# Performance work log

Measured on AMD Instinct MI355X. Metric: run time of the kernel, lower is better.

## Reference

```python
import jax, jax.numpy as jnp
import numpy as np

B, T, D, H = 2, 2048, 1024, 16
DK = D // H


def setup_inputs() -> dict:
    key = jax.random.key(0)
    ks = jax.random.split(key, 9)
    s = 1.0 / np.sqrt(D)
    x = jax.random.normal(ks[0], (B, T, D), dtype=jnp.float32)
    # causal mask (1 = attend, 0 = masked), broadcast over batch and heads
    mask = jnp.tril(jnp.ones((T, T), dtype=jnp.int32))[None, None, :, :]
    Wq = jax.random.uniform(ks[1], (D, D), jnp.float32, -s, s)
    bq = jax.random.uniform(ks[2], (D,), jnp.float32, -s, s)
    Wk = jax.random.uniform(ks[3], (D, D), jnp.float32, -s, s)
    bk = jax.random.uniform(ks[4], (D,), jnp.float32, -s, s)
    Wv = jax.random.uniform(ks[5], (D, D), jnp.float32, -s, s)
    bv = jax.random.uniform(ks[6], (D,), jnp.float32, -s, s)
    Wo = jax.random.uniform(ks[7], (D, D), jnp.float32, -s, s)
    bo = jax.random.uniform(ks[8], (D,), jnp.float32, -s, s)
    return {"x": x, "mask": mask, "Wq": Wq, "bq": bq, "Wk": Wk, "bk": bk,
            "Wv": Wv, "bv": bv, "Wo": Wo, "bo": bo}


def reference(x, mask, Wq, bq, Wk, bk, Wv, bv, Wo, bo):
    # nn.Linear: y = x @ W.T + b
    q = (x @ Wq.T + bq).reshape(B, T, H, DK).transpose(0, 2, 1, 3)  # [B,H,T,DK]
    k = (x @ Wk.T + bk).reshape(B, T, H, DK).transpose(0, 2, 1, 3)
    v = (x @ Wv.T + bv).reshape(B, T, H, DK).transpose(0, 2, 1, 3)
    scores = jnp.einsum('bhqd,bhkd->bhqk', q, k) / np.sqrt(DK).astype(np.float32)
    scores = jnp.where(mask == 0, -jnp.inf, scores)
    attn = jax.nn.softmax(scores, axis=-1)
    out = jnp.einsum('bhqk,bhkd->bhqd', attn, v)  # [B,H,T,DK]
    out = out.transpose(0, 2, 1, 3).reshape(B, T, D)
    return out @ Wo.T + bo
```

## Files before the change

### kernel.cpp

```cpp
#include <hip/hip_runtime.h>

typedef unsigned short u16;
typedef unsigned int u32;
typedef unsigned long long u64;
typedef __attribute__((ext_vector_type(8))) short short8;
typedef __attribute__((ext_vector_type(4))) float f32x4;

#define B_ 2
#define T_ 2048
#define H_ 16
#define DK_ 64
#define QSCALE 0.18033688011112042f

__device__ __forceinline__ u16 f2bf(float f){
  unsigned u = __float_as_uint(f);
  return (u16)((u + 0x7fffu + ((u >> 16) & 1u)) >> 16);
}

__device__ __forceinline__ u32 cvtpk(float lo, float hi){
  u32 r;
  asm("v_cvt_pk_bf16_f32 %0, %1, %2" : "=v"(r) : "v"(lo), "v"(hi));
  return r;
}

#if defined(__has_builtin)
#if __has_builtin(__builtin_amdgcn_global_load_lds)
#define HAS_GLLDS 1
#endif
#if __has_builtin(__builtin_amdgcn_exp2f)
#define EXP2(x) __builtin_amdgcn_exp2f(x)
#endif
#endif
#ifndef EXP2
#define EXP2(x) __expf(0.69314718056f * (x))
#endif

#ifdef HAS_GLLDS
__device__ __forceinline__ void gl_lds16(const u16* g, u16* l){
  __builtin_amdgcn_global_load_lds(
      (__attribute__((address_space(1))) void*)(void*)g,
      (__attribute__((address_space(3))) void*)(void*)l, 16, 0, 0);
}
#endif

__global__ __launch_bounds__(256) void conv_all(
    const float* __restrict__ x, const float* __restrict__ wq, const float* __restrict__ wk,
    const float* __restrict__ wv, const float* __restrict__ wo,
    u16* __restrict__ xb, u16* __restrict__ wqb, u16* __restrict__ wkb,
    u16* __restrict__ wvb, u16* __restrict__ wob)
{
  int gid = blockIdx.x * 256 + threadIdx.x;
  const float* src; u16* dst; int off;
  if (gid < 1048576){ src = x; dst = xb; off = gid; }
  else {
    int t = gid - 1048576; int s = t >> 18; off = t & 262143;
    src = (s==0)?wq:((s==1)?wk:((s==2)?wv:wo));
    dst = (s==0)?wqb:((s==1)?wkb:((s==2)?wvb:wob));
  }
  float4 v = ((const float4*)src)[off];
  u64 r = (u64)f2bf(v.x) | ((u64)f2bf(v.y)<<16) | ((u64)f2bf(v.z)<<32) | ((u64)f2bf(v.w)<<48);
  ((u64*)dst)[off] = r;
}

template<int QKV>
__global__ __launch_bounds__(256, 3) void gemm_k3(
    const u16* __restrict__ A,
    const u16* __restrict__ W0, const u16* __restrict__ W1, const u16* __restrict__ W2,
    const float* __restrict__ b0, const float* __restrict__ b1, const float* __restrict__ b2,
    void* __restrict__ o0, void* __restrict__ o1, void* __restrict__ o2)
{
  __shared__ u16 As[2][128*32];
  __shared__ u16 Bs[2][128*32];
  const int tid = threadIdx.x;
  const int sel = QKV ? (blockIdx.x >> 3) : 0;
  const int n0 = (blockIdx.x & 7) * 128;
  const int m0 = blockIdx.y * 128;
  const u16* Bw = (sel==0)?W0:((sel==1)?W1:W2);
  const float* bias = (sel==0)?b0:((sel==1)?b1:b2);
  const int w = tid>>6, l = tid&63;
  const int lr = l&15, lg = l>>4;
  const int wm = (w&1)*64, wn = (w>>1)*64;
  const u16* Ab = A  + (size_t)m0*1024 + (size_t)(l>>2)*1024 + (l&3)*8;
  const u16* Bb = Bw + (size_t)n0*1024 + (size_t)(l>>2)*1024 + (l&3)*8;
  f32x4 acc[4][4] = {};

#define G_STAGE(k0, pb) do {                                                    \
    _Pragma("unroll")                                                           \
    for (int i_ = 0; i_ < 2; ++i_){                                             \
      int c_ = w*2 + i_;                                                        \
      G_STAGE_ONE(Ab, As, c_, k0, pb); G_STAGE_ONE(Bb, Bs, c_, k0, pb);         \
    } } while(0)
#ifdef HAS_GLLDS
#define G_STAGE_ONE(SRC, DST, c_, k0, pb) \
    gl_lds16(SRC + (size_t)(16*(c_))*1024 + (k0), &DST[pb][(c_)*512])
#else
#define G_STAGE_ONE(SRC, DST, c_, k0, pb) \
    *(uint4*)&DST[pb][(c_)*512 + l*8] = *(const uint4*)(SRC + (size_t)(16*(c_))*1024 + (k0))
#endif

  G_STAGE(0, 0);
  __syncthreads();
  for (int it = 0; it < 32; ++it){
    const int pb = it & 1;
    if (it < 31) G_STAGE((it+1)*32, pb^1);
    short8 af[4], bf[4];
#pragma unroll
    for (int mi=0;mi<4;++mi) af[mi] = *(const short8*)&As[pb][(wm+16*mi+lr)*32 + 8*lg];
#pragma unroll
    for (int ni=0;ni<4;++ni) bf[ni] = *(const short8*)&Bs[pb][(wn+16*ni+lr)*32 + 8*lg];
#pragma unroll
    for (int mi=0;mi<4;++mi)
#pragma unroll
      for (int ni=0;ni<4;++ni)
        acc[mi][ni] = __builtin_amdgcn_mfma_f32_16x16x32_bf16(af[mi], bf[ni], acc[mi][ni], 0,0,0);
    __syncthreads();
  }

  float bv[4];
#pragma unroll
  for (int ni=0;ni<4;++ni) bv[ni] = bias[n0+wn+16*ni+lr];
  void* C = QKV ? ((sel==0)?o0:((sel==1)?o1:o2)) : o0;
#pragma unroll
  for (int mi=0;mi<4;++mi)
#pragma unroll
    for (int r=0;r<4;++r){
      const int trow = m0 + wm + 16*mi + 4*lg + r;
#pragma unroll
      for (int ni=0;ni<4;++ni){
        float v = acc[mi][ni][r] + bv[ni];
        int n = n0 + wn + 16*ni + lr;
        if (!QKV){
          ((float*)C)[(size_t)trow*1024 + n] = v;
        } else if (sel == 0){
          ((u16*)C)[(size_t)trow*1024 + n] = f2bf(v * QSCALE);
        } else if (sel == 1){
          int nsw = (n & ~63) | ((n & 63) ^ ((trow & 7) << 3));
          ((u16*)C)[(size_t)trow*1024 + nsw] = f2bf(v);
        } else {
          ((u16*)C)[(size_t)trow*1024 + n] = f2bf(v);
        }
      }
    }
#undef G_STAGE
#undef G_STAGE_ONE
}

__global__ __launch_bounds__(256) void transpose_v_k(const u16* __restrict__ V,
                                                     u16* __restrict__ VT){
  __shared__ u16 L[64 * 72];
  const int tid = threadIdx.x;
  const int tc = blockIdx.x, h = blockIdx.y, b = blockIdx.z;
#pragma unroll
  for (int p = 0; p < 2; ++p){
    int row = (tid >> 3) + 32 * p, g = tid & 7;
    *(uint4*)&L[row * 72 + g * 8] =
        *(const uint4*)(V + ((size_t)(b * T_ + tc * 64 + row) * H_ + h) * DK_ + g * 8);
  }
  __syncthreads();
#pragma unroll
  for (int p = 0; p < 2; ++p){
    int d = tid >> 2, g8 = (tid & 3) + 4 * p;
    union { uint4 u; u16 s[8]; } tv;
#pragma unroll
    for (int i = 0; i < 8; ++i){
      int pp = 8 * g8 + i;
      int tl = 16 * (pp & 3) + (pp >> 2);
      tv.s[i] = L[tl * 72 + d];
    }
    *(uint4*)(VT + ((size_t)(b * H_ + h) * DK_ + d) * T_ + tc * 64 + ((8 * g8) ^ ((d & 7) << 3))) = tv.u;
  }
}

__global__ __launch_bounds__(256, 2) void attn_v3(
    const u16* __restrict__ Q, const u16* __restrict__ K,
    const u16* __restrict__ VT, u16* __restrict__ O)
{
  __shared__ u16 Ks[2][64*64];
  __shared__ u16 VTs[2][64*64];
  __shared__ u16 Ps[4][32*72];
  const int tid = threadIdx.x;
  const int w = tid>>6, l = tid&63;
  const int lr = l&15, lg = l>>4;
  const int h = blockIdx.y, b = blockIdx.z;
  const int qtb = (b==0) ? blockIdx.x : (15 - blockIdx.x);
  const int q0 = qtb * 128;
  const int wrow0 = q0 + w*32;
  const int sl_r = l>>3, sl_c = (l&7)*8;
  const size_t kbase = ((size_t)(b*T_) * H_ + h) * DK_;
  const size_t vbase = (size_t)(b*H_ + h) * DK_ * (size_t)T_;

#define A_STAGE(kt, pb) do {                                                       \
    _Pragma("unroll")                                                              \
    for (int p_=0;p_<2;++p_){                                                      \
      int r0_ = 8*w + 32*p_;                                                       \
      A_STAGE_K(kt, pb, r0_); A_STAGE_V(kt, pb, r0_);                              \
    } } while(0)
#ifdef HAS_GLLDS
#define A_STAGE_K(kt, pb, r0_) \
    gl_lds16(K  + kbase + (size_t)((kt)*64 + r0_ + sl_r)*1024 + sl_c, &Ks[pb][r0_*64])
#define A_STAGE_V(kt, pb, r0_) \
    gl_lds16(VT + vbase + (size_t)(r0_ + sl_r)*T_ + (kt)*64 + sl_c, &VTs[pb][r0_*64])
#else
#define A_STAGE_K(kt, pb, r0_) \
    *(uint4*)&Ks[pb][(r0_+sl_r)*64 + sl_c] = *(const uint4*)(K + kbase + (size_t)((kt)*64 + r0_ + sl_r)*1024 + sl_c)
#define A_STAGE_V(kt, pb, r0_) \
    *(uint4*)&VTs[pb][(r0_+sl_r)*64 + sl_c] = *(const uint4*)(VT + vbase + (size_t)(r0_ + sl_r)*T_ + (kt)*64 + sl_c)
#endif

  short8 qf[2][2];
#pragma unroll
  for (int mi=0;mi<2;++mi)
#pragma unroll
    for (int s=0;s<2;++s)
      qf[mi][s] = *(const short8*)(Q + kbase + (size_t)(wrow0 + 16*mi + lr)*1024 + s*32 + 8*lg);

  f32x4 acc[2][4] = {};
  float lsum[2][4] = {};
  const int ktend = 2*qtb + 1;

  A_STAGE(0, 0);
  __syncthreads();
  for (int kt = 0; kt <= ktend; ++kt){
    const int pb = kt & 1;
    if (kt < ktend) A_STAGE(kt+1, pb^1);
    if (kt*64 <= wrow0 + 31){
      short8 kf[4][2];
#pragma unroll
      for (int j0=0;j0<4;++j0)
#pragma unroll
        for (int s=0;s<2;++s)
          kf[j0][s] = *(const short8*)&Ks[pb][(j0*16+lr)*64 + (((4*s+lg) ^ (lr&7))<<3)];
      f32x4 sc[2][4];
#pragma unroll
      for (int mi=0;mi<2;++mi)
#pragma unroll
        for (int j0=0;j0<4;++j0){
          f32x4 z = {};
          z = __builtin_amdgcn_mfma_f32_16x16x32_bf16(qf[mi][0], kf[j0][0], z, 0,0,0);
          z = __builtin_amdgcn_mfma_f32_16x16x32_bf16(qf[mi][1], kf[j0][1], z, 0,0,0);
          sc[mi][j0] = z;
        }
      const bool diag = (kt*64 + 63 > wrow0);
#pragma unroll
      for (int mi=0;mi<2;++mi)
#pragma unroll
        for (int r=0;r<4;++r){
          float p0,p1,p2,p3;
          if (diag){
            const int lim = wrow0 + 16*mi + 4*lg + r - kt*64;
            p0 = (lr      <= lim) ? EXP2(sc[mi][0][r]) : 0.f;
            p1 = (16+lr   <= lim) ? EXP2(sc[mi][1][r]) : 0.f;
            p2 = (32+lr   <= lim) ? EXP2(sc[mi][2][r]) : 0.f;
            p3 = (48+lr   <= lim) ? EXP2(sc[mi][3][r]) : 0.f;
          } else {
            p0 = EXP2(sc[mi][0][r]); p1 = EXP2(sc[mi][1][r]);
            p2 = EXP2(sc[mi][2][r]); p3 = EXP2(sc[mi][3][r]);
          }
          lsum[mi][r] += (p0+p1)+(p2+p3);
          u64 pv = (u64)cvtpk(p0,p1) | ((u64)cvtpk(p2,p3) << 32);
          *(u64*)&Ps[w][(16*mi+4*lg+r)*72 + 4*lr] = pv;
        }
#pragma unroll
      for (int ks=0;ks<2;++ks){
        short8 pf0 = *(const short8*)&Ps[w][lr*72      + 32*ks + 8*lg];
        short8 pf1 = *(const short8*)&Ps[w][(16+lr)*72 + 32*ks + 8*lg];
#pragma unroll
        for (int d0=0;d0<4;++d0){
          short8 vf = *(const short8*)&VTs[pb][(d0*16+lr)*64 + (((4*ks+lg) ^ (lr&7))<<3)];
          acc[0][d0] = __builtin_amdgcn_mfma_f32_16x16x32_bf16(pf0, vf, acc[0][d0], 0,0,0);
          acc[1][d0] = __builtin_amdgcn_mfma_f32_16x16x32_bf16(pf1, vf, acc[1][d0], 0,0,0);
        }
      }
    }
    __syncthreads();
  }

#pragma unroll
  for (int mi=0;mi<2;++mi)
#pragma unroll
    for (int r=0;r<4;++r){
      float v = lsum[mi][r];
      v += __shfl_xor(v,1); v += __shfl_xor(v,2);
      v += __shfl_xor(v,4); v += __shfl_xor(v,8);
      lsum[mi][r] = 1.0f / v;
    }
#pragma unroll
  for (int mi=0;mi<2;++mi)
#pragma unroll
    for (int d0=0;d0<4;++d0)
#pragma unroll
      for (int r=0;r<4;++r){
        float ov = acc[mi][d0][r] * lsum[mi][r];
        O[kbase + (size_t)(wrow0 + 16*mi + 4*lg + r)*1024 + d0*16 + lr] = f2bf(ov);
      }
#undef A_STAGE
#undef A_STAGE_K
#undef A_STAGE_V
}

extern "C" void kernel_launch(void* const* d_in, const int* in_sizes, int n_in,
                              void* d_out, int out_size, void* d_ws, size_t ws_size,
                              hipStream_t stream)
{
  const float* x  = (const float*)d_in[0];
  const float* Wq = (const float*)d_in[2];
  const float* bq = (const float*)d_in[3];
  const float* Wk = (const float*)d_in[4];
  const float* bk = (const float*)d_in[5];
  const float* Wv = (const float*)d_in[6];
  const float* bv = (const float*)d_in[7];
  const float* Wo = (const float*)d_in[8];
  const float* bo = (const float*)d_in[9];

  char* ws = (char*)d_ws;
  u16* xb  = (u16*)(ws + 0);
  u16* wqb = (u16*)(ws + 8388608);
  u16* wkb = (u16*)(ws + 10485760);
  u16* wvb = (u16*)(ws + 12582912);
  u16* wob = (u16*)(ws + 14680064);
  u16* qb  = (u16*)(ws + 16777216);
  u16* kb  = (u16*)(ws + 25165824);
  u16* vb  = (u16*)(ws + 33554432);
  u16* vtb = xb;
  u16* ab  = vb;

  conv_all<<<8192, 256, 0, stream>>>(x, Wq, Wk, Wv, Wo, xb, wqb, wkb, wvb, wob);

  gemm_k3<1><<<dim3(24, 32), 256, 0, stream>>>(
      xb, wqb, wkb, wvb, bq, bk, bv, (void*)qb, (void*)kb, (void*)vb);

  transpose_v_k<<<dim3(T_/64, H_, B_), 256, 0, stream>>>(vb, vtb);

  attn_v3<<<dim3(T_/128, H_, B_), 256, 0, stream>>>(qb, kb, vtb, ab);

  gemm_k3<0><<<dim3(8, 32), 256, 0, stream>>>(
      ab, wob, wob, wob, bo, bo, bo, d_out, d_out, d_out);
}
```

Before: 126.3 us.

## Replace LDS-staged attention with direct-from-global K/V fragment loads and smaller tiles

The attention kernel no longer double-buffers K and V^T tiles through shared memory with async global-to-LDS copies and barriers. Each wave now owns 16 query rows and reads K and V^T MFMA fragments straight from global memory, relying on cache for reuse across waves. This drops the XOR swizzle in both the QKV epilogue and the V transpose, halves the query tile to 64 rows per block, doubles the grid, and raises the occupancy hint to 4 blocks per CU. It also switches exp2 to the generic builtin. The cost is more global/L2 traffic per block and exposed load latency with no prefetch, in exchange for no block-wide syncs and higher occupancy.

```diff
diff --git a/kernel.cpp b/kernel.cpp
--- a/kernel.cpp
+++ b/kernel.cpp
@@ -27,13 +27,8 @@
 #if __has_builtin(__builtin_amdgcn_global_load_lds)
 #define HAS_GLLDS 1
 #endif
-#if __has_builtin(__builtin_amdgcn_exp2f)
-#define EXP2(x) __builtin_amdgcn_exp2f(x)
-#endif
-#endif
-#ifndef EXP2
-#define EXP2(x) __expf(0.69314718056f * (x))
-#endif
+#endif
+#define EXP2(x) __builtin_exp2f(x)
 
 #ifdef HAS_GLLDS
 __device__ __forceinline__ void gl_lds16(const u16* g, u16* l){
@@ -133,9 +128,6 @@
           ((float*)C)[(size_t)trow*1024 + n] = v;
         } else if (sel == 0){
           ((u16*)C)[(size_t)trow*1024 + n] = f2bf(v * QSCALE);
-        } else if (sel == 1){
-          int nsw = (n & ~63) | ((n & 63) ^ ((trow & 7) << 3));
-          ((u16*)C)[(size_t)trow*1024 + nsw] = f2bf(v);
         } else {
           ((u16*)C)[(size_t)trow*1024 + n] = f2bf(v);
         }
@@ -167,135 +159,91 @@
       int tl = 16 * (pp & 3) + (pp >> 2);
       tv.s[i] = L[tl * 72 + d];
     }
-    *(uint4*)(VT + ((size_t)(b * H_ + h) * DK_ + d) * T_ + tc * 64 + ((8 * g8) ^ ((d & 7) << 3))) = tv.u;
-  }
-}
-
-__global__ __launch_bounds__(256, 2) void attn_v3(
+    *(uint4*)(VT + ((size_t)(b * H_ + h) * DK_ + d) * T_ + tc * 64 + 8 * g8) = tv.u;
+  }
+}
+
+#define PP 68
+__global__ __launch_bounds__(256, 4) void attn_v4(
     const u16* __restrict__ Q, const u16* __restrict__ K,
     const u16* __restrict__ VT, u16* __restrict__ O)
 {
-  __shared__ u16 Ks[2][64*64];
-  __shared__ u16 VTs[2][64*64];
-  __shared__ u16 Ps[4][32*72];
+  __shared__ u16 Ps[4][16 * PP];
   const int tid = threadIdx.x;
-  const int w = tid>>6, l = tid&63;
-  const int lr = l&15, lg = l>>4;
+  const int w = tid >> 6, l = tid & 63;
+  const int lr = l & 15, lg = l >> 4;
   const int h = blockIdx.y, b = blockIdx.z;
-  const int qtb = (b==0) ? blockIdx.x : (15 - blockIdx.x);
-  const int q0 = qtb * 128;
-  const int wrow0 = q0 + w*32;
-  const int sl_r = l>>3, sl_c = (l&7)*8;
-  const size_t kbase = ((size_t)(b*T_) * H_ + h) * DK_;
-  const size_t vbase = (size_t)(b*H_ + h) * DK_ * (size_t)T_;
-
-#define A_STAGE(kt, pb) do {                                                       \
-    _Pragma("unroll")                                                              \
-    for (int p_=0;p_<2;++p_){                                                      \
-      int r0_ = 8*w + 32*p_;                                                       \
-      A_STAGE_K(kt, pb, r0_); A_STAGE_V(kt, pb, r0_);                              \
-    } } while(0)
-#ifdef HAS_GLLDS
-#define A_STAGE_K(kt, pb, r0_) \
-    gl_lds16(K  + kbase + (size_t)((kt)*64 + r0_ + sl_r)*1024 + sl_c, &Ks[pb][r0_*64])
-#define A_STAGE_V(kt, pb, r0_) \
-    gl_lds16(VT + vbase + (size_t)(r0_ + sl_r)*T_ + (kt)*64 + sl_c, &VTs[pb][r0_*64])
-#else
-#define A_STAGE_K(kt, pb, r0_) \
-    *(uint4*)&Ks[pb][(r0_+sl_r)*64 + sl_c] = *(const uint4*)(K + kbase + (size_t)((kt)*64 + r0_ + sl_r)*1024 + sl_c)
-#define A_STAGE_V(kt, pb, r0_) \
-    *(uint4*)&VTs[pb][(r0_+sl_r)*64 + sl_c] = *(const uint4*)(VT + vbase + (size_t)(r0_ + sl_r)*T_ + (kt)*64 + sl_c)
-#endif
-
-  short8 qf[2][2];
-#pragma unroll
-  for (int mi=0;mi<2;++mi)
-#pragma unroll
-    for (int s=0;s<2;++s)
-      qf[mi][s] = *(const short8*)(Q + kbase + (size_t)(wrow0 + 16*mi + lr)*1024 + s*32 + 8*lg);
-
-  f32x4 acc[2][4] = {};
-  float lsum[2][4] = {};
-  const int ktend = 2*qtb + 1;
-
-  A_STAGE(0, 0);
-  __syncthreads();
-  for (int kt = 0; kt <= ktend; ++kt){
-    const int pb = kt & 1;
-    if (kt < ktend) A_STAGE(kt+1, pb^1);
-    if (kt*64 <= wrow0 + 31){
-      short8 kf[4][2];
-#pragma unroll
-      for (int j0=0;j0<4;++j0)
-#pragma unroll
-        for (int s=0;s<2;++s)
-          kf[j0][s] = *(const short8*)&Ks[pb][(j0*16+lr)*64 + (((4*s+lg) ^ (lr&7))<<3)];
-      f32x4 sc[2][4];
-#pragma unroll
-      for (int mi=0;mi<2;++mi)
-#pragma unroll
-        for (int j0=0;j0<4;++j0){
-          f32x4 z = {};
-          z = __builtin_amdgcn_mfma_f32_16x16x32_bf16(qf[mi][0], kf[j0][0], z, 0,0,0);
-          z = __builtin_amdgcn_mfma_f32_16x16x32_bf16(qf[mi][1], kf[j0][1], z, 0,0,0);
-          sc[mi][j0] = z;
-        }
-      const bool diag = (kt*64 + 63 > wrow0);
-#pragma unroll
-      for (int mi=0;mi<2;++mi)
-#pragma unroll
-        for (int r=0;r<4;++r){
-          float p0,p1,p2,p3;
-          if (diag){
-            const int lim = wrow0 + 16*mi + 4*lg + r - kt*64;
-            p0 = (lr      <= lim) ? EXP2(sc[mi][0][r]) : 0.f;
-            p1 = (16+lr   <= lim) ? EXP2(sc[mi][1][r]) : 0.f;
-            p2 = (32+lr   <= lim) ? EXP2(sc[mi][2][r]) : 0.f;
-            p3 = (48+lr   <= lim) ? EXP2(sc[mi][3][r]) : 0.f;
-          } else {
-            p0 = EXP2(sc[mi][0][r]); p1 = EXP2(sc[mi][1][r]);
-            p2 = EXP2(sc[mi][2][r]); p3 = EXP2(sc[mi][3][r]);
-          }
-          lsum[mi][r] += (p0+p1)+(p2+p3);
-          u64 pv = (u64)cvtpk(p0,p1) | ((u64)cvtpk(p2,p3) << 32);
-          *(u64*)&Ps[w][(16*mi+4*lg+r)*72 + 4*lr] = pv;
-        }
-#pragma unroll
-      for (int ks=0;ks<2;++ks){
-        short8 pf0 = *(const short8*)&Ps[w][lr*72      + 32*ks + 8*lg];
-        short8 pf1 = *(const short8*)&Ps[w][(16+lr)*72 + 32*ks + 8*lg];
-#pragma unroll
-        for (int d0=0;d0<4;++d0){
-          short8 vf = *(const short8*)&VTs[pb][(d0*16+lr)*64 + (((4*ks+lg) ^ (lr&7))<<3)];
-          acc[0][d0] = __builtin_amdgcn_mfma_f32_16x16x32_bf16(pf0, vf, acc[0][d0], 0,0,0);
-          acc[1][d0] = __builtin_amdgcn_mfma_f32_16x16x32_bf16(pf1, vf, acc[1][d0], 0,0,0);
-        }
+  const int qtb = 31 - blockIdx.x;
+  const int wr0 = qtb * 64 + 16 * w;
+  const size_t kbase = ((size_t)(b * T_) * H_ + h) * DK_;
+  const size_t vbase = (size_t)(b * H_ + h) * DK_ * (size_t)T_;
+
+  short8 qf[2];
+#pragma unroll
+  for (int s = 0; s < 2; ++s)
+    qf[s] = *(const short8*)(Q + kbase + (size_t)(wr0 + lr) * 1024 + s * 32 + 8 * lg);
+
+  f32x4 acc[4] = {};
+  float lsum[4] = {};
+
+  for (int kt = 0; kt <= qtb; ++kt){
+    short8 kf[4][2];
+#pragma unroll
+    for (int j0 = 0; j0 < 4; ++j0)
+#pragma unroll
+      for (int s = 0; s < 2; ++s)
+        kf[j0][s] = *(const short8*)(K + kbase + (size_t)(kt * 64 + j0 * 16 + lr) * 1024 + s * 32 + 8 * lg);
+    f32x4 sc[4];
+#pragma unroll
+    for (int j0 = 0; j0 < 4; ++j0){
+      f32x4 z = {};
+      z = __builtin_amdgcn_mfma_f32_16x16x32_bf16(qf[0], kf[j0][0], z, 0, 0, 0);
+      z = __builtin_amdgcn_mfma_f32_16x16x32_bf16(qf[1], kf[j0][1], z, 0, 0, 0);
+      sc[j0] = z;
+    }
+    const bool diag = (kt == qtb);
+#pragma unroll
+    for (int r = 0; r < 4; ++r){
+      float p0, p1, p2, p3;
+      if (diag){
+        const int lim = 16 * w + 4 * lg + r;
+        p0 = (lr      <= lim) ? EXP2(sc[0][r]) : 0.f;
+        p1 = (16 + lr <= lim) ? EXP2(sc[1][r]) : 0.f;
+        p2 = (32 + lr <= lim) ? EXP2(sc[2][r]) : 0.f;
+        p3 = (48 + lr <= lim) ? EXP2(sc[3][r]) : 0.f;
+      } else {
+        p0 = EXP2(sc[0][r]); p1 = EXP2(sc[1][r]);
+        p2 = EXP2(sc[2][r]); p3 = EXP2(sc[3][r]);
       }
-    }
-    __syncthreads();
-  }
-
-#pragma unroll
-  for (int mi=0;mi<2;++mi)
-#pragma unroll
-    for (int r=0;r<4;++r){
-      float v = lsum[mi][r];
-      v += __shfl_xor(v,1); v += __shfl_xor(v,2);
-      v += __shfl_xor(v,4); v += __shfl_xor(v,8);
-      lsum[mi][r] = 1.0f / v;
-    }
-#pragma unroll
-  for (int mi=0;mi<2;++mi)
-#pragma unroll
-    for (int d0=0;d0<4;++d0)
-#pragma unroll
-      for (int r=0;r<4;++r){
-        float ov = acc[mi][d0][r] * lsum[mi][r];
-        O[kbase + (size_t)(wrow0 + 16*mi + 4*lg + r)*1024 + d0*16 + lr] = f2bf(ov);
+      lsum[r] += (p0 + p1) + (p2 + p3);
+      u64 pv = (u64)cvtpk(p0, p1) | ((u64)cvtpk(p2, p3) << 32);
+      *(u64*)&Ps[w][(4 * lg + r) * PP + 4 * lr] = pv;
+    }
+#pragma unroll
+    for (int ks = 0; ks < 2; ++ks){
+      short8 pf = *(const short8*)&Ps[w][lr * PP + 32 * ks + 8 * lg];
+#pragma unroll
+      for (int d0 = 0; d0 < 4; ++d0){
+        short8 vf = *(const short8*)(VT + vbase + (size_t)(d0 * 16 + lr) * T_ + kt * 64 + 32 * ks + 8 * lg);
+        acc[d0] = __builtin_amdgcn_mfma_f32_16x16x32_bf16(pf, vf, acc[d0], 0, 0, 0);
       }
-#undef A_STAGE
-#undef A_STAGE_K
-#undef A_STAGE_V
+    }
+  }
+
+#pragma unroll
+  for (int r = 0; r < 4; ++r){
+    float v = lsum[r];
+    v += __shfl_xor(v, 1); v += __shfl_xor(v, 2);
+    v += __shfl_xor(v, 4); v += __shfl_xor(v, 8);
+    lsum[r] = 1.0f / v;
+  }
+#pragma unroll
+  for (int d0 = 0; d0 < 4; ++d0)
+#pragma unroll
+    for (int r = 0; r < 4; ++r){
+      float ov = acc[d0][r] * lsum[r];
+      O[kbase + (size_t)(wr0 + 4 * lg + r) * 1024 + d0 * 16 + lr] = f2bf(ov);
+    }
 }
 
 extern "C" void kernel_launch(void* const* d_in, const int* in_sizes, int n_in,
@@ -331,7 +279,7 @@
 
   transpose_v_k<<<dim3(T_/64, H_, B_), 256, 0, stream>>>(vb, vtb);
 
-  attn_v3<<<dim3(T_/128, H_, B_), 256, 0, stream>>>(qb, kb, vtb, ab);
+  attn_v4<<<dim3(T_/64, H_, B_), 256, 0, stream>>>(qb, kb, vtb, ab);
 
   gemm_k3<0><<<dim3(8, 32), 256, 0, stream>>>(
       ab, wob, wob, wob, bo, bo, bo, d_out, d_out, d_out);
```

After: 303.1 us. +139.9%, slower.

## Triple-buffer LDS staging with partial vmcnt waits in GEMM and attention

Applied to the files above, without the earlier changes.

Both the projection GEMM and the attention kernel move from double-buffered to triple-buffered LDS staging, issuing loads two tiles ahead. Each loop iteration now waits with s_waitcnt vmcnt(4) so the newest tile's loads can stay in flight, then uses a raw s_barrier instead of __syncthreads. This targets memory latency that the single-tile lookahead leaves exposed, at the cost of more LDS per block, which may reduce occupancy. The exp2 macro is also switched to __builtin_exp2f.

```diff
diff --git a/kernel.cpp b/kernel.cpp
--- a/kernel.cpp
+++ b/kernel.cpp
@@ -23,16 +23,12 @@
   return r;
 }
 
+#define EXP2(x) __builtin_exp2f(x)
+
 #if defined(__has_builtin)
 #if __has_builtin(__builtin_amdgcn_global_load_lds)
 #define HAS_GLLDS 1
 #endif
-#if __has_builtin(__builtin_amdgcn_exp2f)
-#define EXP2(x) __builtin_amdgcn_exp2f(x)
-#endif
-#endif
-#ifndef EXP2
-#define EXP2(x) __expf(0.69314718056f * (x))
 #endif
 
 #ifdef HAS_GLLDS
@@ -41,6 +37,17 @@
       (__attribute__((address_space(1))) void*)(void*)g,
       (__attribute__((address_space(3))) void*)(void*)l, 16, 0, 0);
 }
+__device__ __forceinline__ void wait_vm4(){ asm volatile("s_waitcnt vmcnt(4)" ::: "memory"); }
+__device__ __forceinline__ void wait_vm0(){ asm volatile("s_waitcnt vmcnt(0)" ::: "memory"); }
+__device__ __forceinline__ void pipe_bar(){
+  asm volatile("" ::: "memory");
+  __builtin_amdgcn_s_barrier();
+  asm volatile("" ::: "memory");
+}
+#else
+__device__ __forceinline__ void wait_vm4(){}
+__device__ __forceinline__ void wait_vm0(){}
+__device__ __forceinline__ void pipe_bar(){ __syncthreads(); }
 #endif
 
 __global__ __launch_bounds__(256) void conv_all(
@@ -63,14 +70,14 @@
 }
 
 template<int QKV>
-__global__ __launch_bounds__(256, 3) void gemm_k3(
+__global__ __launch_bounds__(256, 3) void gemm_k5(
     const u16* __restrict__ A,
     const u16* __restrict__ W0, const u16* __restrict__ W1, const u16* __restrict__ W2,
     const float* __restrict__ b0, const float* __restrict__ b1, const float* __restrict__ b2,
     void* __restrict__ o0, void* __restrict__ o1, void* __restrict__ o2)
 {
-  __shared__ u16 As[2][128*32];
-  __shared__ u16 Bs[2][128*32];
+  __shared__ u16 As[3 * 4096];
+  __shared__ u16 Bs[3 * 4096];
   const int tid = threadIdx.x;
   const int sel = QKV ? (blockIdx.x >> 3) : 0;
   const int n0 = (blockIdx.x & 7) * 128;
@@ -84,36 +91,41 @@
   const u16* Bb = Bw + (size_t)n0*1024 + (size_t)(l>>2)*1024 + (l&3)*8;
   f32x4 acc[4][4] = {};
 
-#define G_STAGE(k0, pb) do {                                                    \
-    _Pragma("unroll")                                                           \
-    for (int i_ = 0; i_ < 2; ++i_){                                             \
-      int c_ = w*2 + i_;                                                        \
-      G_STAGE_ONE(Ab, As, c_, k0, pb); G_STAGE_ONE(Bb, Bs, c_, k0, pb);         \
-    } } while(0)
+  auto STAGE = [&](int t, int pb){
+#pragma unroll
+    for (int i = 0; i < 2; ++i){
+      int c = w*2 + i;
 #ifdef HAS_GLLDS
-#define G_STAGE_ONE(SRC, DST, c_, k0, pb) \
-    gl_lds16(SRC + (size_t)(16*(c_))*1024 + (k0), &DST[pb][(c_)*512])
+      gl_lds16(Ab + (size_t)(16*c)*1024 + t*32, &As[pb*4096 + c*512]);
+      gl_lds16(Bb + (size_t)(16*c)*1024 + t*32, &Bs[pb*4096 + c*512]);
 #else
-#define G_STAGE_ONE(SRC, DST, c_, k0, pb) \
-    *(uint4*)&DST[pb][(c_)*512 + l*8] = *(const uint4*)(SRC + (size_t)(16*(c_))*1024 + (k0))
-#endif
-
-  G_STAGE(0, 0);
-  __syncthreads();
+      *(uint4*)&As[pb*4096 + c*512 + l*8] = *(const uint4*)(Ab + (size_t)(16*c)*1024 + t*32);
+      *(uint4*)&Bs[pb*4096 + c*512 + l*8] = *(const uint4*)(Bb + (size_t)(16*c)*1024 + t*32);
+#endif
+    }
+  };
+
+  STAGE(0, 0); STAGE(1, 1);
+  wait_vm4();
+  pipe_bar();
   for (int it = 0; it < 32; ++it){
-    const int pb = it & 1;
-    if (it < 31) G_STAGE((it+1)*32, pb^1);
+    const int pb = it % 3;
+    if (it < 30) STAGE(it + 2, (it + 2) % 3);
     short8 af[4], bf[4];
 #pragma unroll
-    for (int mi=0;mi<4;++mi) af[mi] = *(const short8*)&As[pb][(wm+16*mi+lr)*32 + 8*lg];
-#pragma unroll
-    for (int ni=0;ni<4;++ni) bf[ni] = *(const short8*)&Bs[pb][(wn+16*ni+lr)*32 + 8*lg];
+    for (int mi=0;mi<4;++mi) af[mi] = *(const short8*)&As[pb*4096 + (wm+16*mi+lr)*32 + 8*lg];
+#pragma unroll
+    for (int ni=0;ni<4;++ni) bf[ni] = *(const short8*)&Bs[pb*4096 + (wn+16*ni+lr)*32 + 8*lg];
 #pragma unroll
     for (int mi=0;mi<4;++mi)
 #pragma unroll
       for (int ni=0;ni<4;++ni)
         acc[mi][ni] = __builtin_amdgcn_mfma_f32_16x16x32_bf16(af[mi], bf[ni], acc[mi][ni], 0,0,0);
-    __syncthreads();
+    if (it < 31){
+      if (it < 30) wait_vm4();
+      else         wait_vm0();
+      pipe_bar();
+    }
   }
 
   float bv[4];
@@ -141,8 +153,6 @@
         }
       }
     }
-#undef G_STAGE
-#undef G_STAGE_ONE
 }
 
 __global__ __launch_bounds__(256) void transpose_v_k(const u16* __restrict__ V,
@@ -171,13 +181,13 @@
   }
 }
 
-__global__ __launch_bounds__(256, 2) void attn_v3(
+__global__ __launch_bounds__(256, 2) void attn_v5(
     const u16* __restrict__ Q, const u16* __restrict__ K,
     const u16* __restrict__ VT, u16* __restrict__ O)
 {
-  __shared__ u16 Ks[2][64*64];
-  __shared__ u16 VTs[2][64*64];
-  __shared__ u16 Ps[4][32*72];
+  __shared__ u16 Ks[3 * 4096];
+  __shared__ u16 VTs[3 * 4096];
+  __shared__ u16 Ps[4][32 * 72];
   const int tid = threadIdx.x;
   const int w = tid>>6, l = tid&63;
   const int lr = l&15, lg = l>>4;
@@ -189,23 +199,21 @@
   const size_t kbase = ((size_t)(b*T_) * H_ + h) * DK_;
   const size_t vbase = (size_t)(b*H_ + h) * DK_ * (size_t)T_;
 
-#define A_STAGE(kt, pb) do {                                                       \
-    _Pragma("unroll")                                                              \
-    for (int p_=0;p_<2;++p_){                                                      \
-      int r0_ = 8*w + 32*p_;                                                       \
-      A_STAGE_K(kt, pb, r0_); A_STAGE_V(kt, pb, r0_);                              \
-    } } while(0)
+  auto STAGE = [&](int kt, int pb){
+#pragma unroll
+    for (int p=0;p<2;++p){
+      int r0 = 8*w + 32*p;
 #ifdef HAS_GLLDS
-#define A_STAGE_K(kt, pb, r0_) \
-    gl_lds16(K  + kbase + (size_t)((kt)*64 + r0_ + sl_r)*1024 + sl_c, &Ks[pb][r0_*64])
-#define A_STAGE_V(kt, pb, r0_) \
-    gl_lds16(VT + vbase + (size_t)(r0_ + sl_r)*T_ + (kt)*64 + sl_c, &VTs[pb][r0_*64])
+      gl_lds16(K  + kbase + (size_t)(kt*64 + r0 + sl_r)*1024 + sl_c, &Ks[pb*4096 + r0*64]);
+      gl_lds16(VT + vbase + (size_t)(r0 + sl_r)*T_ + kt*64 + sl_c, &VTs[pb*4096 + r0*64]);
 #else
-#define A_STAGE_K(kt, pb, r0_) \
-    *(uint4*)&Ks[pb][(r0_+sl_r)*64 + sl_c] = *(const uint4*)(K + kbase + (size_t)((kt)*64 + r0_ + sl_r)*1024 + sl_c)
-#define A_STAGE_V(kt, pb, r0_) \
-    *(uint4*)&VTs[pb][(r0_+sl_r)*64 + sl_c] = *(const uint4*)(VT + vbase + (size_t)(r0_ + sl_r)*T_ + (kt)*64 + sl_c)
-#endif
+      *(uint4*)&Ks[pb*4096 + (r0+sl_r)*64 + sl_c] =
+          *(const uint4*)(K + kbase + (size_t)(kt*64 + r0 + sl_r)*1024 + sl_c);
+      *(uint4*)&VTs[pb*4096 + (r0+sl_r)*64 + sl_c] =
+          *(const uint4*)(VT + vbase + (size_t)(r0 + sl_r)*T_ + kt*64 + sl_c);
+#endif
+    }
+  };
 
   short8 qf[2][2];
 #pragma unroll
@@ -218,18 +226,20 @@
   float lsum[2][4] = {};
   const int ktend = 2*qtb + 1;
 
-  A_STAGE(0, 0);
-  __syncthreads();
+  STAGE(0, 0); STAGE(1, 1);
+  wait_vm4();
+  pipe_bar();
   for (int kt = 0; kt <= ktend; ++kt){
-    const int pb = kt & 1;
-    if (kt < ktend) A_STAGE(kt+1, pb^1);
+    const int pb = kt % 3;
+    const bool more2 = (kt + 2 <= ktend);
+    if (more2) STAGE(kt + 2, (kt + 2) % 3);
     if (kt*64 <= wrow0 + 31){
       short8 kf[4][2];
 #pragma unroll
       for (int j0=0;j0<4;++j0)
 #pragma unroll
         for (int s=0;s<2;++s)
-          kf[j0][s] = *(const short8*)&Ks[pb][(j0*16+lr)*64 + (((4*s+lg) ^ (lr&7))<<3)];
+          kf[j0][s] = *(const short8*)&Ks[pb*4096 + (j0*16+lr)*64 + (((4*s+lg) ^ (lr&7))<<3)];
       f32x4 sc[2][4];
 #pragma unroll
       for (int mi=0;mi<2;++mi)
@@ -266,13 +276,17 @@
         short8 pf1 = *(const short8*)&Ps[w][(16+lr)*72 + 32*ks + 8*lg];
 #pragma unroll
         for (int d0=0;d0<4;++d0){
-          short8 vf = *(const short8*)&VTs[pb][(d0*16+lr)*64 + (((4*ks+lg) ^ (lr&7))<<3)];
+          short8 vf = *(const short8*)&VTs[pb*4096 + (d0*16+lr)*64 + (((4*ks+lg) ^ (lr&7))<<3)];
           acc[0][d0] = __builtin_amdgcn_mfma_f32_16x16x32_bf16(pf0, vf, acc[0][d0], 0,0,0);
           acc[1][d0] = __builtin_amdgcn_mfma_f32_16x16x32_bf16(pf1, vf, acc[1][d0], 0,0,0);
         }
       }
     }
-    __syncthreads();
+    if (kt < ktend){
+      if (more2) wait_vm4();
+      else       wait_vm0();
+      pipe_bar();
+    }
   }
 
 #pragma unroll
@@ -293,9 +307,6 @@
         float ov = acc[mi][d0][r] * lsum[mi][r];
         O[kbase + (size_t)(wrow0 + 16*mi + 4*lg + r)*1024 + d0*16 + lr] = f2bf(ov);
       }
-#undef A_STAGE
-#undef A_STAGE_K
-#undef A_STAGE_V
 }
 
 extern "C" void kernel_launch(void* const* d_in, const int* in_sizes, int n_in,
@@ -326,13 +337,13 @@
 
   conv_all<<<8192, 256, 0, stream>>>(x, Wq, Wk, Wv, Wo, xb, wqb, wkb, wvb, wob);
 
-  gemm_k3<1><<<dim3(24, 32), 256, 0, stream>>>(
+  gemm_k5<1><<<dim3(24, 32), 256, 0, stream>>>(
       xb, wqb, wkb, wvb, bq, bk, bv, (void*)qb, (void*)kb, (void*)vb);
 
   transpose_v_k<<<dim3(T_/64, H_, B_), 256, 0, stream>>>(vb, vtb);
 
-  attn_v3<<<dim3(T_/128, H_, B_), 256, 0, stream>>>(qb, kb, vtb, ab);
-
-  gemm_k3<0><<<dim3(8, 32), 256, 0, stream>>>(
+  attn_v5<<<dim3(T_/128, H_, B_), 256, 0, stream>>>(qb, kb, vtb, ab);
+
+  gemm_k5<0><<<dim3(8, 32), 256, 0, stream>>>(
       ab, wob, wob, wob, bo, bo, bo, d_out, d_out, d_out);
 }
```

Measured after the change: 137.3 us. 1.09x slower.
